# Performance work log

Measured on AMD Instinct MI355X. Metric: run time of the kernel, lower is better.

## Reference

```python
import jax, jax.numpy as jnp
import numpy as np

NUM_HEADS = 32
NUM_KV_HEADS = 8
HEAD_DIM = 128
SCALE = 0.08838834764831845  # 1/sqrt(128)
NUM_SEQS = 8
BLKS_PER_SEQ = 64
MEM_BLOCK_SIZE = 32          # ctx_len = 64*32 = 2048 per sequence
Q_LEN = 64                   # active diffusion block per sequence
N_BLOCKS = 1024


def setup_inputs() -> dict:
    key = jax.random.key(0)
    k1, k2, k3, k4, k5 = jax.random.split(key, 5)
    T = NUM_SEQS * Q_LEN
    q = jax.random.normal(k1, (T, NUM_HEADS * HEAD_DIM), dtype=jnp.float32)
    k = jax.random.normal(k2, (T, NUM_KV_HEADS * HEAD_DIM), dtype=jnp.float32)
    v = jax.random.normal(k3, (T, NUM_KV_HEADS * HEAD_DIM), dtype=jnp.float32)
    k_cache = jax.random.normal(k4, (N_BLOCKS, MEM_BLOCK_SIZE, NUM_KV_HEADS, HEAD_DIM), dtype=jnp.float32)
    v_cache = jax.random.normal(k5, (N_BLOCKS, MEM_BLOCK_SIZE, NUM_KV_HEADS, HEAD_DIM), dtype=jnp.float32)
    # each sequence owns a distinct contiguous set of cache blocks
    block_tables = jnp.arange(NUM_SEQS * BLKS_PER_SEQ, dtype=jnp.int32).reshape(NUM_SEQS, BLKS_PER_SEQ)
    return {"q": q, "k": k, "v": v, "k_cache": k_cache, "v_cache": v_cache,
            "block_tables": block_tables}


def reference(q, k, v, k_cache, v_cache, block_tables):
    S, B = block_tables.shape
    ctx_len = B * MEM_BLOCK_SIZE
    G = NUM_HEADS // NUM_KV_HEADS  # GQA group size

    # reshape flattened token streams: [T, H*D] -> [S, L, H, D]
    qh = q.reshape(S, Q_LEN, NUM_KV_HEADS, G, HEAD_DIM)
    kn = k.reshape(S, Q_LEN, NUM_KV_HEADS, HEAD_DIM)
    vn = v.reshape(S, Q_LEN, NUM_KV_HEADS, HEAD_DIM)

    # paged gather: block_tables -> [S, B, MEM_BLK, Hkv, D] -> [S, ctx_len, Hkv, D]
    kc = k_cache[block_tables].reshape(S, ctx_len, NUM_KV_HEADS, HEAD_DIM)
    vc = v_cache[block_tables].reshape(S, ctx_len, NUM_KV_HEADS, HEAD_DIM)

    # packed KV = gathered context ++ new active-block tokens (load_kvcache kernel)
    K = jnp.concatenate([kc, kn], axis=1)  # [S, ctx_len+Q_LEN, Hkv, D]
    V = jnp.concatenate([vc, vn], axis=1)

    # diffusion-LM mask: active block attends bidirectionally to full context + itself
    scores = jnp.einsum('sqhgd,skhd->shgqk', qh, K) * SCALE
    probs = jax.nn.softmax(scores, axis=-1)
    out = jnp.einsum('shgqk,skhd->sqhgd', probs, V)
    return out.reshape(S * Q_LEN, NUM_HEADS * HEAD_DIM)
```

## Files before the change

### kernel.cpp

```cpp
#include <hip/hip_runtime.h>

#define NUM_HEADS 32
#define NUM_KV_HEADS 8
#define HEAD_DIM 128
#define GQA 4
#define NUM_SEQS 8
#define BLKS_PER_SEQ 64
#define MEM_BLK 32
#define Q_LEN 64
#define SCALE 0.08838834764831845f
#define RLN2 1.4426950408889634f

typedef __attribute__((ext_vector_type(4))) float f4;
typedef __attribute__((ext_vector_type(4))) float f32x4;
typedef __attribute__((ext_vector_type(8))) short short8;
typedef __attribute__((ext_vector_type(4))) unsigned int u32x4;

__device__ __forceinline__ unsigned cvt_pk(float lo, float hi) {
  unsigned r;
  asm("v_cvt_pk_bf16_f32 %0, %1, %2" : "=v"(r) : "v"(lo), "v"(hi));
  return r;
}
__device__ __forceinline__ unsigned short f2bf(float f) {
  unsigned int u = __builtin_bit_cast(unsigned int, f);
  u += 0x7fffu + ((u >> 16) & 1u);
  return (unsigned short)(u >> 16);
}

#define K_OFF   0
#define V_OFF   16384
#define P_OFF   32768
#define ML_OFF  43008
#define BT_OFF  43520
#define LDS_BYTES 43776

__device__ __forceinline__ unsigned k_addr(int key, int d) {
  return (unsigned)(key * 256 + ((d * 2) ^ ((key & 7) << 4)));
}
__device__ __forceinline__ unsigned v_addr(int d, int key) {
  return (unsigned)(d * 64 + ((key * 2) ^ (((d >> 2) & 3) << 4)));
}

__global__ __launch_bounds__(512, 2)
void attn_paged_kernel(const float* __restrict__ q, const float* __restrict__ kn,
                       const float* __restrict__ vn, const float* __restrict__ kc,
                       const float* __restrict__ vc, const int* __restrict__ btab,
                       float* __restrict__ out)
{
  __shared__ __align__(16) char lds[LDS_BYTES];

  const int bid = blockIdx.x;
  const int sh  = bid & 63;
  const int g   = bid >> 6;
  const int s   = sh >> 3;
  const int h   = sh & 7;
  const int tid  = threadIdx.x;
  const int wave = tid >> 6, lane = tid & 63;
  const int rg  = wave & 3;
  const int par = wave >> 2;
  const int lhi = lane >> 4, llo = lane & 15;

  if (tid < 64) *(int*)(lds + BT_OFF + tid * 4) = btab[s * BLKS_PER_SEQ + tid];

  short8 qf[4];
  {
    const float qsc = SCALE * RLN2;
    const float* qrow = q + (size_t)(s * Q_LEN + rg * 16 + llo) * 4096 + (h * GQA + g) * 128;
#pragma unroll
    for (int c = 0; c < 4; ++c) {
      const float* p = qrow + c * 32 + lhi * 8;
      f4 a = *(const f4*)p;
      f4 b = *(const f4*)(p + 4);
      u32x4 w;
      w[0] = cvt_pk(a[0] * qsc, a[1] * qsc);
      w[1] = cvt_pk(a[2] * qsc, a[3] * qsc);
      w[2] = cvt_pk(b[0] * qsc, b[1] * qsc);
      w[3] = cvt_pk(b[2] * qsc, b[3] * qsc);
      qf[c] = __builtin_bit_cast(short8, w);
    }
  }

  f32x4 of[8];
#pragma unroll
  for (int i = 0; i < 8; ++i) of[i] = (f32x4){0.f, 0.f, 0.f, 0.f};
  float m_run[4], l_run[4];
#pragma unroll
  for (int r = 0; r < 4; ++r) { m_run[r] = -1e30f; l_run[r] = 0.f; }

  const int ktk = tid >> 4;
  const int kc0 = (tid & 15) * 8;
  const int vcq = tid & 31;
  const int vtp = tid >> 5;
  const size_t k_toff  = (size_t)ktk * 1024 + h * HEAD_DIM + kc0;
  const size_t v_toff0 = (size_t)(2 * vtp) * 1024 + h * HEAD_DIM + vcq * 4;
  char* kw  = lds + K_OFF + k_addr(ktk, kc0);
  char* vw0 = lds + V_OFF + v_addr(vcq * 4, 2 * vtp);

  __syncthreads();

  f4 rka[2], rkb[2], rva[2], rvb[2];

  auto issue_loads = [&](int it_next) {
#pragma unroll
    for (int pp = 0; pp < 2; ++pp) {
      const int tile = 2 * it_next + pp;
      const float *kb_, *vb_;
      if (tile < BLKS_PER_SEQ) {
        const int pb = *(const int*)(lds + BT_OFF + tile * 4);
        kb_ = kc + (size_t)pb * 32768;
        vb_ = vc + (size_t)pb * 32768;
      } else {
        const size_t row = (size_t)(s * Q_LEN + (tile - BLKS_PER_SEQ) * MEM_BLK) * 1024;
        kb_ = kn + row;
        vb_ = vn + row;
      }
      rka[pp] = *(const f4*)(kb_ + k_toff);
      rkb[pp] = *(const f4*)(kb_ + k_toff + 4);
      rva[pp] = *(const f4*)(vb_ + v_toff0);
      rvb[pp] = *(const f4*)(vb_ + v_toff0 + 1024);
    }
  };
  auto write_tiles = [&]() {
#pragma unroll
    for (int pp = 0; pp < 2; ++pp) {
      u32x4 w;
      w[0] = cvt_pk(rka[pp][0], rka[pp][1]);
      w[1] = cvt_pk(rka[pp][2], rka[pp][3]);
      w[2] = cvt_pk(rkb[pp][0], rkb[pp][1]);
      w[3] = cvt_pk(rkb[pp][2], rkb[pp][3]);
      *(u32x4*)(kw + pp * 8192) = w;
#pragma unroll
      for (int i = 0; i < 4; ++i)
        *(unsigned*)(vw0 + pp * 8192 + i * 64) = cvt_pk(rva[pp][i], rvb[pp][i]);
    }
  };

  issue_loads(0);
  write_tiles();
  __syncthreads();

  for (int it = 0; it < 33; ++it) {
    if (it < 32) issue_loads(it + 1);

    {
      const char* kb  = lds + K_OFF + par * 8192;
      const char* vbp = lds + V_OFF + par * 8192;
      f32x4 s0 = {0.f, 0.f, 0.f, 0.f}, s1 = {0.f, 0.f, 0.f, 0.f};
#pragma unroll
      for (int c = 0; c < 4; ++c) {
        short8 kf0 = *(const short8*)(kb + k_addr(llo,      c * 32 + lhi * 8));
        short8 kf1 = *(const short8*)(kb + k_addr(llo + 16, c * 32 + lhi * 8));
        s0 = __builtin_amdgcn_mfma_f32_16x16x32_bf16(qf[c], kf0, s0, 0, 0, 0);
        s1 = __builtin_amdgcn_mfma_f32_16x16x32_bf16(qf[c], kf1, s1, 0, 0, 0);
      }
      float p0[4], p1[4], tred[4];
#pragma unroll
      for (int r = 0; r < 4; ++r) tred[r] = fmaxf(s0[r], s1[r]);
#pragma unroll
      for (int off = 1; off < 16; off <<= 1)
#pragma unroll
        for (int r = 0; r < 4; ++r) tred[r] = fmaxf(tred[r], __shfl_xor(tred[r], off, 64));

      bool grow = (tred[0] > m_run[0]) | (tred[1] > m_run[1]) |
                  (tred[2] > m_run[2]) | (tred[3] > m_run[3]);
      const int resc = __any((int)grow);
      float corr[4];
      if (resc) {
#pragma unroll
        for (int r = 0; r < 4; ++r) {
          const float mnew = fmaxf(m_run[r], tred[r]);
          corr[r] = exp2f(m_run[r] - mnew);
          m_run[r] = mnew;
        }
      }
#pragma unroll
      for (int r = 0; r < 4; ++r) {
        p0[r] = exp2f(s0[r] - m_run[r]);
        p1[r] = exp2f(s1[r] - m_run[r]);
        tred[r] = p0[r] + p1[r];
      }
#pragma unroll
      for (int off = 1; off < 16; off <<= 1)
#pragma unroll
        for (int r = 0; r < 4; ++r) tred[r] += __shfl_xor(tred[r], off, 64);
      if (resc) {
#pragma unroll
        for (int r = 0; r < 4; ++r) l_run[r] = l_run[r] * corr[r] + tred[r];
#pragma unroll
        for (int dc = 0; dc < 8; ++dc)
#pragma unroll
          for (int r = 0; r < 4; ++r) of[dc][r] *= corr[r];
      } else {
#pragma unroll
        for (int r = 0; r < 4; ++r) l_run[r] += tred[r];
      }

      char* pb_ = lds + P_OFF + wave * 1280;
#pragma unroll
      for (int r = 0; r < 4; ++r) {
        const int row = lhi * 4 + r;
        *(unsigned short*)(pb_ + row * 80 + llo * 2)        = f2bf(p0[r]);
        *(unsigned short*)(pb_ + row * 80 + (llo + 16) * 2) = f2bf(p1[r]);
      }
      short8 pa = *(const short8*)(pb_ + llo * 80 + lhi * 16);
#pragma unroll
      for (int dc = 0; dc < 8; ++dc) {
        short8 vf = *(const short8*)(vbp + v_addr(dc * 16 + llo, lhi * 8));
        of[dc] = __builtin_amdgcn_mfma_f32_16x16x32_bf16(pa, vf, of[dc], 0, 0, 0);
      }
    }

    __syncthreads();
    if (it < 32) write_tiles();
    __syncthreads();
  }

  if (par == 1) {
    char* mo = lds + rg * 8192;
#pragma unroll
    for (int dc = 0; dc < 8; ++dc)
#pragma unroll
      for (int r = 0; r < 4; ++r)
        *(float*)(mo + (lhi * 4 + r) * 512 + (dc * 16 + llo) * 4) = of[dc][r];
    if (llo == 0) {
      char* ml = lds + ML_OFF + rg * 128;
#pragma unroll
      for (int r = 0; r < 4; ++r) {
        *(float*)(ml + (lhi * 4 + r) * 8)     = m_run[r];
        *(float*)(ml + (lhi * 4 + r) * 8 + 4) = l_run[r];
      }
    }
  }
  __syncthreads();
  if (par == 0) {
    const char* mo = lds + rg * 8192;
    const char* ml = lds + ML_OFF + rg * 128;
    float ca[4], cb[4], inv[4];
#pragma unroll
    for (int r = 0; r < 4; ++r) {
      const float mb = *(const float*)(ml + (lhi * 4 + r) * 8);
      const float lb = *(const float*)(ml + (lhi * 4 + r) * 8 + 4);
      const float mf = fmaxf(m_run[r], mb);
      ca[r] = exp2f(m_run[r] - mf);
      cb[r] = exp2f(mb - mf);
      inv[r] = 1.f / (ca[r] * l_run[r] + cb[r] * lb);
    }
#pragma unroll
    for (int dc = 0; dc < 8; ++dc)
#pragma unroll
      for (int r = 0; r < 4; ++r) {
        const float ob = *(const float*)(mo + (lhi * 4 + r) * 512 + (dc * 16 + llo) * 4);
        const float val = (ca[r] * of[dc][r] + cb[r] * ob) * inv[r];
        out[(size_t)(s * Q_LEN + rg * 16 + lhi * 4 + r) * 4096
            + (size_t)((h * GQA + g) * 128 + dc * 16 + llo)] = val;
      }
  }
}

extern "C" void kernel_launch(void* const* d_in, const int* in_sizes, int n_in,
                              void* d_out, int out_size, void* d_ws, size_t ws_size,
                              hipStream_t stream) {
  (void)in_sizes; (void)n_in; (void)d_ws; (void)ws_size; (void)out_size;
  const float* q  = (const float*)d_in[0];
  const float* k  = (const float*)d_in[1];
  const float* v  = (const float*)d_in[2];
  const float* kc = (const float*)d_in[3];
  const float* vc = (const float*)d_in[4];
  const int* bt   = (const int*)d_in[5];
  float* out = (float*)d_out;
  attn_paged_kernel<<<dim3(256), dim3(512), 0, stream>>>(q, k, v, kc, vc, bt, out);
}
```

Before: 300.8 us.

## Split KV sequence across workgroups with global partial results and merge kernel

Replaces the intra-block two-parity split (512 threads, 256 blocks) with a split-KV scheme: the 66 KV tiles are divided across up to 4 chunks, each handled by a 256-thread workgroup, giving up to 1024 workgroups. Partial outputs and m/l statistics go to workspace, and a separate merge kernel combines them. The aim is more parallelism and occupancy on a 256-CU GPU where 256 blocks underfill the machine. The cost is an extra kernel launch plus global traffic for the partials, and the chunk count silently depends on the workspace size.

```diff
diff --git a/kernel.cpp b/kernel.cpp
--- a/kernel.cpp
+++ b/kernel.cpp
@@ -1,15 +1,11 @@
 #include <hip/hip_runtime.h>
 
-#define NUM_HEADS 32
-#define NUM_KV_HEADS 8
-#define HEAD_DIM 128
 #define GQA 4
-#define NUM_SEQS 8
-#define BLKS_PER_SEQ 64
-#define MEM_BLK 32
 #define Q_LEN 64
 #define SCALE 0.08838834764831845f
 #define RLN2 1.4426950408889634f
+#define NTILES 66
+#define CACHE_TILES 64
 
 typedef __attribute__((ext_vector_type(4))) float f4;
 typedef __attribute__((ext_vector_type(4))) float f32x4;
@@ -22,61 +18,58 @@
   return r;
 }
 __device__ __forceinline__ unsigned short f2bf(float f) {
-  unsigned int u = __builtin_bit_cast(unsigned int, f);
+  unsigned u = __builtin_bit_cast(unsigned, f);
   u += 0x7fffu + ((u >> 16) & 1u);
   return (unsigned short)(u >> 16);
 }
 
-#define K_OFF   0
-#define V_OFF   16384
-#define P_OFF   32768
-#define ML_OFF  43008
-#define BT_OFF  43520
-#define LDS_BYTES 43776
+#define K_OFF  0
+#define V_OFF  8192
+#define P_OFF  18432
+#define BT_OFF 23552
+#define LDS_BYTES 23808
 
 __device__ __forceinline__ unsigned k_addr(int key, int d) {
   return (unsigned)(key * 256 + ((d * 2) ^ ((key & 7) << 4)));
 }
 __device__ __forceinline__ unsigned v_addr(int d, int key) {
-  return (unsigned)(d * 64 + ((key * 2) ^ (((d >> 2) & 3) << 4)));
-}
-
-__global__ __launch_bounds__(512, 2)
-void attn_paged_kernel(const float* __restrict__ q, const float* __restrict__ kn,
-                       const float* __restrict__ vn, const float* __restrict__ kc,
-                       const float* __restrict__ vc, const int* __restrict__ btab,
-                       float* __restrict__ out)
+  return (unsigned)(d * 80 + key * 2);
+}
+
+__global__ __launch_bounds__(256, 4)
+void attn_partial(const float* __restrict__ q, const float* __restrict__ kn,
+                  const float* __restrict__ vn, const float* __restrict__ kc,
+                  const float* __restrict__ vc, const int* __restrict__ btab,
+                  float* __restrict__ part_o, float* __restrict__ part_ml,
+                  float* __restrict__ out, int nc)
 {
   __shared__ __align__(16) char lds[LDS_BYTES];
-
-  const int bid = blockIdx.x;
-  const int sh  = bid & 63;
-  const int g   = bid >> 6;
-  const int s   = sh >> 3;
-  const int h   = sh & 7;
+  const int bid  = blockIdx.x;
+  const int c    = bid >> 8;
+  const int rest = bid & 255;
+  const int g = rest >> 6, s = (rest >> 3) & 7, h = rest & 7;
   const int tid  = threadIdx.x;
   const int wave = tid >> 6, lane = tid & 63;
-  const int rg  = wave & 3;
-  const int par = wave >> 2;
-  const int lhi = lane >> 4, llo = lane & 15;
-
-  if (tid < 64) *(int*)(lds + BT_OFF + tid * 4) = btab[s * BLKS_PER_SEQ + tid];
+  const int lhi  = lane >> 4, llo = lane & 15;
+
+  const int base  = NTILES / nc, rem = NTILES % nc;
+  const int start = c * base + (c < rem ? c : rem);
+  const int nt    = base + (c < rem ? 1 : 0);
+
+  if (tid < 64) *(int*)(lds + BT_OFF + tid * 4) = btab[s * CACHE_TILES + tid];
 
   short8 qf[4];
   {
     const float qsc = SCALE * RLN2;
-    const float* qrow = q + (size_t)(s * Q_LEN + rg * 16 + llo) * 4096 + (h * GQA + g) * 128;
-#pragma unroll
-    for (int c = 0; c < 4; ++c) {
-      const float* p = qrow + c * 32 + lhi * 8;
-      f4 a = *(const f4*)p;
-      f4 b = *(const f4*)(p + 4);
+    const float* qrow = q + (size_t)(s * Q_LEN + wave * 16 + llo) * 4096 + (h * GQA + g) * 128;
+#pragma unroll
+    for (int cc = 0; cc < 4; ++cc) {
+      const float* p = qrow + cc * 32 + lhi * 8;
+      f4 a = *(const f4*)p; f4 b = *(const f4*)(p + 4);
       u32x4 w;
-      w[0] = cvt_pk(a[0] * qsc, a[1] * qsc);
-      w[1] = cvt_pk(a[2] * qsc, a[3] * qsc);
-      w[2] = cvt_pk(b[0] * qsc, b[1] * qsc);
-      w[3] = cvt_pk(b[2] * qsc, b[3] * qsc);
-      qf[c] = __builtin_bit_cast(short8, w);
+      w[0] = cvt_pk(a[0] * qsc, a[1] * qsc); w[1] = cvt_pk(a[2] * qsc, a[3] * qsc);
+      w[2] = cvt_pk(b[0] * qsc, b[1] * qsc); w[3] = cvt_pk(b[2] * qsc, b[3] * qsc);
+      qf[cc] = __builtin_bit_cast(short8, w);
     }
   }
 
@@ -87,71 +80,65 @@
 #pragma unroll
   for (int r = 0; r < 4; ++r) { m_run[r] = -1e30f; l_run[r] = 0.f; }
 
-  const int ktk = tid >> 4;
-  const int kc0 = (tid & 15) * 8;
-  const int vcq = tid & 31;
-  const int vtp = tid >> 5;
-  const size_t k_toff  = (size_t)ktk * 1024 + h * HEAD_DIM + kc0;
-  const size_t v_toff0 = (size_t)(2 * vtp) * 1024 + h * HEAD_DIM + vcq * 4;
-  char* kw  = lds + K_OFF + k_addr(ktk, kc0);
-  char* vw0 = lds + V_OFF + v_addr(vcq * 4, 2 * vtp);
+  const int ktk = tid >> 3;
+  const int kc0 = (tid & 7) * 16;
+  const int vdq = (tid >> 3) * 4;
+  const int vkp = tid & 7;
+  const size_t k_toff = (size_t)ktk * 1024 + h * 128 + kc0;
+  const size_t v_off0 = (size_t)(2 * vkp) * 1024 + h * 128 + vdq;
+
+  f4 rk[4], rv[4];
+  auto issue_loads = [&](int tile) {
+    const float *kb_, *vb_;
+    if (tile < CACHE_TILES) {
+      const int pb = *(const int*)(lds + BT_OFF + tile * 4);
+      kb_ = kc + (size_t)pb * 32768;
+      vb_ = vc + (size_t)pb * 32768;
+    } else {
+      const size_t row0 = (size_t)(s * Q_LEN + (tile - CACHE_TILES) * 32) * 1024;
+      kb_ = kn + row0;
+      vb_ = vn + row0;
+    }
+    rk[0] = *(const f4*)(kb_ + k_toff);
+    rk[1] = *(const f4*)(kb_ + k_toff + 4);
+    rk[2] = *(const f4*)(kb_ + k_toff + 8);
+    rk[3] = *(const f4*)(kb_ + k_toff + 12);
+    rv[0] = *(const f4*)(vb_ + v_off0);
+    rv[1] = *(const f4*)(vb_ + v_off0 + 1024);
+    rv[2] = *(const f4*)(vb_ + v_off0 + 16384);
+    rv[3] = *(const f4*)(vb_ + v_off0 + 17408);
+  };
+  auto write_tile = [&]() {
+    u32x4 w0, w1;
+    w0[0] = cvt_pk(rk[0][0], rk[0][1]); w0[1] = cvt_pk(rk[0][2], rk[0][3]);
+    w0[2] = cvt_pk(rk[1][0], rk[1][1]); w0[3] = cvt_pk(rk[1][2], rk[1][3]);
+    w1[0] = cvt_pk(rk[2][0], rk[2][1]); w1[1] = cvt_pk(rk[2][2], rk[2][3]);
+    w1[2] = cvt_pk(rk[3][0], rk[3][1]); w1[3] = cvt_pk(rk[3][2], rk[3][3]);
+    *(u32x4*)(lds + K_OFF + k_addr(ktk, kc0))     = w0;
+    *(u32x4*)(lds + K_OFF + k_addr(ktk, kc0 + 8)) = w1;
+#pragma unroll
+    for (int i = 0; i < 4; ++i) {
+      *(unsigned*)(lds + V_OFF + v_addr(vdq + i, 2 * vkp))      = cvt_pk(rv[0][i], rv[1][i]);
+      *(unsigned*)(lds + V_OFF + v_addr(vdq + i, 2 * vkp + 16)) = cvt_pk(rv[2][i], rv[3][i]);
+    }
+  };
 
   __syncthreads();
-
-  f4 rka[2], rkb[2], rva[2], rvb[2];
-
-  auto issue_loads = [&](int it_next) {
-#pragma unroll
-    for (int pp = 0; pp < 2; ++pp) {
-      const int tile = 2 * it_next + pp;
-      const float *kb_, *vb_;
-      if (tile < BLKS_PER_SEQ) {
-        const int pb = *(const int*)(lds + BT_OFF + tile * 4);
-        kb_ = kc + (size_t)pb * 32768;
-        vb_ = vc + (size_t)pb * 32768;
-      } else {
-        const size_t row = (size_t)(s * Q_LEN + (tile - BLKS_PER_SEQ) * MEM_BLK) * 1024;
-        kb_ = kn + row;
-        vb_ = vn + row;
-      }
-      rka[pp] = *(const f4*)(kb_ + k_toff);
-      rkb[pp] = *(const f4*)(kb_ + k_toff + 4);
-      rva[pp] = *(const f4*)(vb_ + v_toff0);
-      rvb[pp] = *(const f4*)(vb_ + v_toff0 + 1024);
-    }
-  };
-  auto write_tiles = [&]() {
-#pragma unroll
-    for (int pp = 0; pp < 2; ++pp) {
-      u32x4 w;
-      w[0] = cvt_pk(rka[pp][0], rka[pp][1]);
-      w[1] = cvt_pk(rka[pp][2], rka[pp][3]);
-      w[2] = cvt_pk(rkb[pp][0], rkb[pp][1]);
-      w[3] = cvt_pk(rkb[pp][2], rkb[pp][3]);
-      *(u32x4*)(kw + pp * 8192) = w;
-#pragma unroll
-      for (int i = 0; i < 4; ++i)
-        *(unsigned*)(vw0 + pp * 8192 + i * 64) = cvt_pk(rva[pp][i], rvb[pp][i]);
-    }
-  };
-
-  issue_loads(0);
-  write_tiles();
+  issue_loads(start);
+  write_tile();
   __syncthreads();
 
-  for (int it = 0; it < 33; ++it) {
-    if (it < 32) issue_loads(it + 1);
+  for (int it = 0; it < nt; ++it) {
+    if (it + 1 < nt) issue_loads(start + it + 1);
 
     {
-      const char* kb  = lds + K_OFF + par * 8192;
-      const char* vbp = lds + V_OFF + par * 8192;
-      f32x4 s0 = {0.f, 0.f, 0.f, 0.f}, s1 = {0.f, 0.f, 0.f, 0.f};
-#pragma unroll
-      for (int c = 0; c < 4; ++c) {
-        short8 kf0 = *(const short8*)(kb + k_addr(llo,      c * 32 + lhi * 8));
-        short8 kf1 = *(const short8*)(kb + k_addr(llo + 16, c * 32 + lhi * 8));
-        s0 = __builtin_amdgcn_mfma_f32_16x16x32_bf16(qf[c], kf0, s0, 0, 0, 0);
-        s1 = __builtin_amdgcn_mfma_f32_16x16x32_bf16(qf[c], kf1, s1, 0, 0, 0);
+      f32x4 s0 = {0.f,0.f,0.f,0.f}, s1 = {0.f,0.f,0.f,0.f};
+#pragma unroll
+      for (int cc = 0; cc < 4; ++cc) {
+        short8 kf0 = *(const short8*)(lds + K_OFF + k_addr(llo,      cc * 32 + lhi * 8));
+        short8 kf1 = *(const short8*)(lds + K_OFF + k_addr(llo + 16, cc * 32 + lhi * 8));
+        s0 = __builtin_amdgcn_mfma_f32_16x16x32_bf16(qf[cc], kf0, s0, 0, 0, 0);
+        s1 = __builtin_amdgcn_mfma_f32_16x16x32_bf16(qf[cc], kf1, s1, 0, 0, 0);
       }
       float p0[4], p1[4], tred[4];
 #pragma unroll
@@ -205,62 +192,84 @@
       short8 pa = *(const short8*)(pb_ + llo * 80 + lhi * 16);
 #pragma unroll
       for (int dc = 0; dc < 8; ++dc) {
-        short8 vf = *(const short8*)(vbp + v_addr(dc * 16 + llo, lhi * 8));
+        short8 vf = *(const short8*)(lds + V_OFF + v_addr(dc * 16 + llo, lhi * 8));
         of[dc] = __builtin_amdgcn_mfma_f32_16x16x32_bf16(pa, vf, of[dc], 0, 0, 0);
       }
     }
 
     __syncthreads();
-    if (it < 32) write_tiles();
-    __syncthreads();
-  }
-
-  if (par == 1) {
-    char* mo = lds + rg * 8192;
+    if (it + 1 < nt) {
+      write_tile();
+      __syncthreads();
+    }
+  }
+
+  if (nc == 1) {
+    float inv[4];
+#pragma unroll
+    for (int r = 0; r < 4; ++r) inv[r] = 1.f / l_run[r];
 #pragma unroll
     for (int dc = 0; dc < 8; ++dc)
 #pragma unroll
       for (int r = 0; r < 4; ++r)
-        *(float*)(mo + (lhi * 4 + r) * 512 + (dc * 16 + llo) * 4) = of[dc][r];
+        out[(size_t)(s * Q_LEN + wave * 16 + lhi * 4 + r) * 4096
+            + (size_t)((h * GQA + g) * 128 + dc * 16 + llo)] = of[dc][r] * inv[r];
+  } else {
+#pragma unroll
+    for (int dc = 0; dc < 8; ++dc)
+#pragma unroll
+      for (int r = 0; r < 4; ++r) {
+        const int row = wave * 16 + lhi * 4 + r;
+        part_o[((size_t)bid * 64 + row) * 128 + dc * 16 + llo] = of[dc][r];
+      }
     if (llo == 0) {
-      char* ml = lds + ML_OFF + rg * 128;
-#pragma unroll
-      for (int r = 0; r < 4; ++r) {
-        *(float*)(ml + (lhi * 4 + r) * 8)     = m_run[r];
-        *(float*)(ml + (lhi * 4 + r) * 8 + 4) = l_run[r];
-      }
-    }
-  }
-  __syncthreads();
-  if (par == 0) {
-    const char* mo = lds + rg * 8192;
-    const char* ml = lds + ML_OFF + rg * 128;
-    float ca[4], cb[4], inv[4];
-#pragma unroll
-    for (int r = 0; r < 4; ++r) {
-      const float mb = *(const float*)(ml + (lhi * 4 + r) * 8);
-      const float lb = *(const float*)(ml + (lhi * 4 + r) * 8 + 4);
-      const float mf = fmaxf(m_run[r], mb);
-      ca[r] = exp2f(m_run[r] - mf);
-      cb[r] = exp2f(mb - mf);
-      inv[r] = 1.f / (ca[r] * l_run[r] + cb[r] * lb);
-    }
-#pragma unroll
-    for (int dc = 0; dc < 8; ++dc)
-#pragma unroll
-      for (int r = 0; r < 4; ++r) {
-        const float ob = *(const float*)(mo + (lhi * 4 + r) * 512 + (dc * 16 + llo) * 4);
-        const float val = (ca[r] * of[dc][r] + cb[r] * ob) * inv[r];
-        out[(size_t)(s * Q_LEN + rg * 16 + lhi * 4 + r) * 4096
-            + (size_t)((h * GQA + g) * 128 + dc * 16 + llo)] = val;
-      }
-  }
+#pragma unroll
+      for (int r = 0; r < 4; ++r) {
+        const int row = wave * 16 + lhi * 4 + r;
+        part_ml[(size_t)bid * 128 + row]      = m_run[r];
+        part_ml[(size_t)bid * 128 + 64 + row] = l_run[r];
+      }
+    }
+  }
+}
+
+template<int NC>
+__global__ __launch_bounds__(256)
+void merge_k(const float* __restrict__ po, const float* __restrict__ pml,
+             float* __restrict__ out)
+{
+  const int t   = blockIdx.x * 256 + threadIdx.x;
+  const int d4  = t & 31;
+  const int hh  = (t >> 5) & 31;
+  const int tok = t >> 10;
+  const int s = tok >> 6, row = tok & 63, h = hh >> 2, g = hh & 3;
+
+  float m[NC], l[NC]; f4 o[NC];
+  float M = -1e30f;
+#pragma unroll
+  for (int c = 0; c < NC; ++c) {
+    const int bid = c * 256 + g * 64 + s * 8 + h;
+    m[c] = pml[(size_t)bid * 128 + row];
+    l[c] = pml[(size_t)bid * 128 + 64 + row];
+    o[c] = *(const f4*)&po[((size_t)bid * 64 + row) * 128 + d4 * 4];
+    M = fmaxf(M, m[c]);
+  }
+  f4 num = {0.f,0.f,0.f,0.f};
+  float den = 0.f;
+#pragma unroll
+  for (int c = 0; c < NC; ++c) {
+    const float w = exp2f(m[c] - M);
+    num += w * o[c];
+    den += w * l[c];
+  }
+  const float inv = 1.f / den;
+  *(f4*)&out[(size_t)tok * 4096 + hh * 128 + d4 * 4] = num * inv;
 }
 
 extern "C" void kernel_launch(void* const* d_in, const int* in_sizes, int n_in,
                               void* d_out, int out_size, void* d_ws, size_t ws_size,
                               hipStream_t stream) {
-  (void)in_sizes; (void)n_in; (void)d_ws; (void)ws_size; (void)out_size;
+  (void)in_sizes; (void)n_in; (void)out_size;
   const float* q  = (const float*)d_in[0];
   const float* k  = (const float*)d_in[1];
   const float* v  = (const float*)d_in[2];
@@ -268,5 +277,16 @@
   const float* vc = (const float*)d_in[4];
   const int* bt   = (const int*)d_in[5];
   float* out = (float*)d_out;
-  attn_paged_kernel<<<dim3(256), dim3(512), 0, stream>>>(q, k, v, kc, vc, bt, out);
-}
+
+  const size_t per_chunk = 256ull * 64 * 128 * 4 + 256ull * 128 * 4;
+  int NC = 1;
+  if (ws_size >= 4 * per_chunk) NC = 4;
+  else if (ws_size >= 2 * per_chunk) NC = 2;
+
+  float* po  = (float*)d_ws;
+  float* pml = po + (size_t)NC * 256 * 64 * 128;
+
+  attn_partial<<<dim3(NC * 256), dim3(256), 0, stream>>>(q, k, v, kc, vc, bt, po, pml, out, NC);
+  if (NC == 4)      merge_k<4><<<dim3(2048), dim3(256), 0, stream>>>(po, pml, out);
+  else if (NC == 2) merge_k<2><<<dim3(2048), dim3(256), 0, stream>>>(po, pml, out);
+}
```

After: 302.6 us. Within noise of the previous version (+0.6%).
